# Kernel optimization log

Measured on AMD Instinct MI355X. Metric: run time of the kernel, lower is better.

Reference implementation:

```python
import jax, jax.numpy as jnp
import numpy as np

LSTM_IN = 125
LSTM_H = 125
MLP_D_H = 512
N = 512


def _lstm_scan(x, Wih, Whh, bih, bhh):
    # x: (N, LSTM_IN); PyTorch gate order: i, f, g, o
    H = LSTM_H
    def step(carry, xt):
        h, c = carry
        g = Wih @ xt + Whh @ h + bih + bhh  # (4H,)
        i = jax.nn.sigmoid(g[:H])
        f = jax.nn.sigmoid(g[H:2 * H])
        gg = jnp.tanh(g[2 * H:3 * H])
        o = jax.nn.sigmoid(g[3 * H:])
        c = f * c + i * gg
        h = o * jnp.tanh(c)
        return (h, c), h
    init = (jnp.zeros((H,), x.dtype), jnp.zeros((H,), x.dtype))
    _, hs = jax.lax.scan(step, init, x)
    return hs  # (N, H)


def setup_inputs() -> dict:
    key = jax.random.key(0)
    ks = jax.random.split(key, 14)
    s = 0.05
    d = {
        "sentence_emb": jax.random.normal(ks[0], (N, 1, LSTM_IN), jnp.float32),
        "Wih_f": jax.random.normal(ks[1], (4 * LSTM_H, LSTM_IN), jnp.float32) * s,
        "Whh_f": jax.random.normal(ks[2], (4 * LSTM_H, LSTM_H), jnp.float32) * s,
        "bih_f": jax.random.normal(ks[3], (4 * LSTM_H,), jnp.float32) * s,
        "bhh_f": jax.random.normal(ks[4], (4 * LSTM_H,), jnp.float32) * s,
        "Wih_b": jax.random.normal(ks[5], (4 * LSTM_H, LSTM_IN), jnp.float32) * s,
        "Whh_b": jax.random.normal(ks[6], (4 * LSTM_H, LSTM_H), jnp.float32) * s,
        "bih_b": jax.random.normal(ks[7], (4 * LSTM_H,), jnp.float32) * s,
        "bhh_b": jax.random.normal(ks[8], (4 * LSTM_H,), jnp.float32) * s,
        "W1": jax.random.normal(ks[9], (MLP_D_H, 4 * LSTM_H), jnp.float32) * s,
        "b1": jax.random.normal(ks[10], (MLP_D_H,), jnp.float32) * s,
        "W2": jax.random.normal(ks[11], (1, MLP_D_H), jnp.float32) * s,
        "b2": jax.random.normal(ks[12], (1,), jnp.float32) * s,
    }
    return d


def reference(sentence_emb, Wih_f, Whh_f, bih_f, bhh_f, Wih_b, Whh_b, bih_b, bhh_b, W1, b1, W2, b2):
    x = sentence_emb[:, 0, :]  # (N, 125), batch=1
    h_fwd = _lstm_scan(x, Wih_f, Whh_f, bih_f, bhh_f)           # (N, 125)
    h_bwd = _lstm_scan(x[::-1], Wih_b, Whh_b, bih_b, bhh_b)[::-1]  # (N, 125)
    h = jnp.concatenate([h_fwd, h_bwd], axis=-1)  # (N, 250)
    # output_mtx[i, j] = MLP(concat(h[j], h[i]))
    # Decompose first linear: W1 @ cat(h_j, h_i) = Wa @ h_j + Wb @ h_i
    D = h.shape[-1]
    Pa = h @ W1[:, :D].T   # (N, H): contribution of h_j
    Pb = h @ W1[:, D:].T   # (N, H): contribution of h_i
    hidden = jnp.tanh(Pb[:, None, :] + Pa[None, :, :] + b1)  # (N, N, H)
    out = hidden @ W2[0] + b2[0]  # (N, N)
    return out
```

## Files before the change

### kernel.cpp

```cpp
#include <hip/hip_runtime.h>

typedef __bf16 bf16_t;
typedef __bf16 bf16x8 __attribute__((ext_vector_type(8)));
typedef float f32x4 __attribute__((ext_vector_type(4)));
typedef int   int4v __attribute__((ext_vector_type(4)));

#define LOG2E 1.4426950408889634f

template<int CTRL>
__device__ __forceinline__ float qperm(float x) {
  return __builtin_bit_cast(float,
      __builtin_amdgcn_update_dpp(0, __builtin_bit_cast(int, x), CTRL, 0xF, 0xF, true));
}

__device__ __forceinline__ void lds_barrier() {
  asm volatile("s_waitcnt lgkmcnt(0)\n\ts_barrier" ::: "memory");
}

#if __has_builtin(__builtin_amdgcn_sdot4)
__device__ __forceinline__ int DOT4(int a, int b, int c) {
  return __builtin_amdgcn_sdot4(a, b, c, false);
}
#else
__device__ __forceinline__ int DOT4(int a, int b, int c) {
  #pragma unroll
  for (int i = 0; i < 4; ++i)
    c += ((a << (24 - 8 * i)) >> 24) * ((b << (24 - 8 * i)) >> 24);
  return c;
}
#endif

__global__ __launch_bounds__(256) void pre_kernel(
    const float* __restrict__ x,
    const float* __restrict__ Wih_f, const float* __restrict__ bih_f,
    const float* __restrict__ bhh_f,
    const float* __restrict__ Wih_b, const float* __restrict__ bih_b,
    const float* __restrict__ bhh_b,
    float* __restrict__ preT)
{
  const int dir = blockIdx.x >> 5;
  const int T   = blockIdx.x & 31;
  const float* __restrict__ Wih = dir ? Wih_b : Wih_f;
  const float* __restrict__ bih = dir ? bih_b : bih_f;
  const float* __restrict__ bhh = dir ? bhh_b : bhh_f;

  const int tid = threadIdx.x;
  const int wv  = tid >> 6;
  const int lane = tid & 63;
  const int q = lane >> 4, cc = lane & 15;

  const int r  = 16 * T + cc;
  const int na = r >> 2, pa = r & 3;
  const bool vld = (na < 125);
  const float* __restrict__ Wr = Wih + (vld ? (125 * pa + na) * 125 : 0);

  bf16x8 whi[4], wlo[4];
  #pragma unroll
  for (int ks = 0; ks < 4; ++ks) {
    #pragma unroll
    for (int j = 0; j < 8; ++j) {
      int k = 32 * ks + 8 * q + j;
      float wvv = (vld && k < 125) ? Wr[k] : 0.0f;
      bf16_t hi = (bf16_t)wvv;
      whi[ks][j] = hi;
      wlo[ks][j] = (bf16_t)(wvv - (float)hi);
    }
  }

  float bias[4];
  #pragma unroll
  for (int reg = 0; reg < 4; ++reg) {
    int ro = 16 * T + 4 * q + reg;
    int no = ro >> 2, po = ro & 3;
    bias[reg] = (no < 125) ? (bih[125 * po + no] + bhh[125 * po + no]) : 0.0f;
  }

  for (int i = 0; i < 8; ++i) {
    const int tt = 8 * wv + i;
    const int t  = 16 * tt + cc;
    const int trow = dir ? (511 - t) : t;
    const float* __restrict__ xr = x + trow * 125;

    f32x4 acc = (f32x4)0.0f;
    #pragma unroll
    for (int ks = 0; ks < 4; ++ks) {
      bf16x8 xhi, xlo;
      #pragma unroll
      for (int j = 0; j < 8; ++j) {
        int k = 32 * ks + 8 * q + j;
        float xv = (k < 125) ? xr[k] : 0.0f;
        bf16_t hi = (bf16_t)xv;
        xhi[j] = hi;
        xlo[j] = (bf16_t)(xv - (float)hi);
      }
      acc = __builtin_amdgcn_mfma_f32_16x16x32_bf16(whi[ks], xhi, acc, 0, 0, 0);
      acc = __builtin_amdgcn_mfma_f32_16x16x32_bf16(whi[ks], xlo, acc, 0, 0, 0);
      acc = __builtin_amdgcn_mfma_f32_16x16x32_bf16(wlo[ks], xhi, acc, 0, 0, 0);
    }
    #pragma unroll
    for (int reg = 0; reg < 4; ++reg) {
      int ro = 16 * T + 4 * q + reg;
      preT[dir * 262144 + ro * 512 + 16 * tt + cc] = acc[reg] + bias[reg];
    }
  }
}

__global__ __launch_bounds__(512) void lstm_kernel(
    const float* __restrict__ Whh_f, const float* __restrict__ Whh_b,
    const float* __restrict__ pre,
    bf16_t* __restrict__ h_all)
{
  const int dir = blockIdx.x;
  const float* __restrict__ Whh = dir ? Whh_b : Whh_f;

  const int tid  = threadIdx.x;
  const int lane = tid & 63;
  const int w    = tid >> 6;
  const int n    = tid >> 2;
  const int p    = tid & 3;
  const bool vld = (n < 125);
  const float* __restrict__ Wrow = Whh + (vld ? (125 * p + n) * 125 : 0);

  float m0 = 0.f, m1 = 0.f, m2 = 0.f, m3 = 0.f;
  if (vld) {
    #pragma unroll 4
    for (int k = 0; k < 124; k += 4) {
      m0 = fmaxf(m0, fabsf(Wrow[k + 0]));
      m1 = fmaxf(m1, fabsf(Wrow[k + 1]));
      m2 = fmaxf(m2, fabsf(Wrow[k + 2]));
      m3 = fmaxf(m3, fabsf(Wrow[k + 3]));
    }
    m0 = fmaxf(m0, fabsf(Wrow[124]));
  }
  float wm = fmaxf(fmaxf(m0, m1), fmaxf(m2, m3));
  #pragma unroll
  for (int off = 1; off < 64; off <<= 1)
    wm = fmaxf(wm, __shfl_xor(wm, off));
  __shared__ float wmx[8];
  if (lane == 0) wmx[w] = wm;
  __syncthreads();
  float wmax = wmx[0];
  #pragma unroll
  for (int u = 1; u < 8; ++u) wmax = fmaxf(wmax, wmx[u]);
  const float s_w  = 127.0f / wmax;
  const float invq = wmax / (127.0f * 127.0f);

  int wq[32];
  #pragma unroll
  for (int word = 0; word < 32; ++word) {
    int b = 0;
    #pragma unroll
    for (int byte = 0; byte < 4; ++byte) {
      int k = 4 * word + byte;
      int qv = 0;
      if (vld && k < 125)
        qv = (int)__builtin_rintf(Wrow[k] * s_w);
      b |= (qv & 0xFF) << (8 * byte);
    }
    wq[word] = b;
  }

  __shared__ __align__(16) char hbuf[2][128];
  if (tid < 256) ((char*)hbuf)[tid] = 0;
  if (dir == 0) {
    #pragma unroll
    for (int u = 0; u < 6; ++u) h_all[tid * 256 + 250 + u] = (bf16_t)0.0f;
  }
  __syncthreads();

  const float mult   = (p == 2) ? (-2.0f * LOG2E) : (-LOG2E);
  const float sA     = (p == 2) ? 2.0f : 1.0f;
  const float sB     = (p == 2) ? -1.0f : 0.0f;
  const float dscale = mult * invq;
  const float* __restrict__ preR = pre + dir * 262144 + tid * 512;
  float c = 0.0f;

  float4 pv_cur = *(const float4*)preR;

  for (int g = 0; g < 128; ++g) {
    float4 pv_nxt = make_float4(0.f, 0.f, 0.f, 0.f);
    if (g < 127) pv_nxt = *(const float4*)(preR + 4 * (g + 1));

    #pragma unroll
    for (int s4 = 0; s4 < 4; ++s4) {
      const int step = 4 * g + s4;
      const int cur  = s4 & 1, nxt = cur ^ 1;
      const float pv = (s4 == 0) ? pv_cur.x : (s4 == 1) ? pv_cur.y
                     : (s4 == 2) ? pv_cur.z : pv_cur.w;
      const float pvm = mult * pv;

      int hv[32];
      #pragma unroll
      for (int j = 0; j < 8; ++j) {
        int4v v = *(const int4v*)&hbuf[cur][16 * j];
        hv[4 * j + 0] = v[0];
        hv[4 * j + 1] = v[1];
        hv[4 * j + 2] = v[2];
        hv[4 * j + 3] = v[3];
      }

      int d0 = 0, d1 = 0, d2 = 0, d3 = 0;
      #pragma unroll
      for (int j = 0; j < 8; ++j) {
        d0 = DOT4(wq[4 * j + 0], hv[4 * j + 0], d0);
        d1 = DOT4(wq[4 * j + 1], hv[4 * j + 1], d1);
        d2 = DOT4(wq[4 * j + 2], hv[4 * j + 2], d2);
        d3 = DOT4(wq[4 * j + 3], hv[4 * j + 3], d3);
      }
      const int D = (d0 + d1) + (d2 + d3);

      float gf  = (float)D;
      float xg  = fmaf(gf, dscale, pvm);
      float e   = __builtin_amdgcn_exp2f(xg);
      float y   = __builtin_amdgcn_rcpf(1.0f + e);
      float act = fmaf(y, sA, sB);

      float b_i = qperm<0x00>(act);
      float b_f = qperm<0x55>(act);
      float b_g = qperm<0xAA>(act);
      float b_o = qperm<0xFF>(act);
      c = fmaf(b_f, c, b_i * b_g);
      float e2 = __builtin_amdgcn_exp2f(-2.0f * LOG2E * c);
      float tc = fmaf(__builtin_amdgcn_rcpf(1.0f + e2), 2.0f, -1.0f);
      float h  = b_o * tc;

      if (p == 0) {
        int qh = (int)__builtin_rintf(h * 127.0f);
        hbuf[nxt][n] = (char)qh;
        if (n < 125) {
          int t_orig = dir ? (511 - step) : step;
          h_all[t_orig * 256 + dir * 125 + n] = (bf16_t)h;
        }
      }
      lds_barrier();
    }
    pv_cur = pv_nxt;
  }
}

__global__ __launch_bounds__(256) void qgemm_kernel(
    const bf16_t* __restrict__ h_all,
    const float* __restrict__ W1,
    const float* __restrict__ b1,
    float* __restrict__ Qa,
    float* __restrict__ Qb)
{
  const int tid  = threadIdx.x;
  const int wv   = tid >> 6;
  const int lane = tid & 63;
  const int q    = lane >> 4, cc = lane & 15;
  const int bj   = blockIdx.x & 31;
  const int bm   = blockIdx.x >> 5;
  const int m    = bm * 64 + wv * 16 + cc;
  const int j0   = bj * 16;
  const int jA   = j0 + cc;

  const bool isB = (m >= 512);
  const int  row = isB ? (m - 512) : m;
  const int  cof = isB ? 250 : 0;

  f32x4 acc = (f32x4)0.0f;
  #pragma unroll
  for (int ks = 0; ks < 8; ++ks) {
    int kb = 32 * ks + 8 * q;
    bf16x8 a = *(const bf16x8*)&h_all[jA * 256 + kb];
    bf16x8 b;
    #pragma unroll
    for (int jj = 0; jj < 8; ++jj) {
      int k = kb + jj;
      float v = (k < 250) ? W1[row * 500 + cof + k] : 0.0f;
      b[jj] = (bf16_t)v;
    }
    acc = __builtin_amdgcn_mfma_f32_16x16x32_bf16(a, b, acc, 0, 0, 0);
  }

  const float C2 = 2.0f * LOG2E;
  #pragma unroll
  for (int reg = 0; reg < 4; ++reg) {
    int j = j0 + 4 * q + reg;
    float v = acc[reg];
    if (!isB) Qa[j * 512 + m] = C2 * v;
    else      Qb[j * 512 + (m - 512)] = C2 * (v + b1[m - 512]);
  }
}

__global__ __launch_bounds__(256) void outer_kernel(
    const float* __restrict__ Qa, const float* __restrict__ Qb,
    const float* __restrict__ W2, const float* __restrict__ b2,
    float* __restrict__ out)
{
  __shared__ float sa[2][32][33];
  __shared__ float sb[2][32][33];
  __shared__ float sw[2][32];

  const int tid = threadIdx.x;
  const int bi  = blockIdx.x >> 4, bjx = blockIdx.x & 15;
  const int i0  = bi * 32, j0 = bjx * 32;
  const int ii0 = (tid & 15) * 2;
  const int jj0 = (tid >> 4) * 2;
  const int ljj = tid & 31, kk4 = (tid >> 5) * 4;

  float accR[2][2] = {{0.0f, 0.0f}, {0.0f, 0.0f}};
  float wsum = 0.0f;

  for (int kc = 0; kc < 16; ++kc) {
    const int buf = kc & 1;
    const int k0  = kc * 32;
    float4 va = *(const float4*)&Qa[(j0 + ljj) * 512 + k0 + kk4];
    float4 vb = *(const float4*)&Qb[(i0 + ljj) * 512 + k0 + kk4];
    sa[buf][kk4 + 0][ljj] = va.x; sa[buf][kk4 + 1][ljj] = va.y;
    sa[buf][kk4 + 2][ljj] = va.z; sa[buf][kk4 + 3][ljj] = va.w;
    sb[buf][kk4 + 0][ljj] = vb.x; sb[buf][kk4 + 1][ljj] = vb.y;
    sb[buf][kk4 + 2][ljj] = vb.z; sb[buf][kk4 + 3][ljj] = vb.w;
    if (tid < 32) sw[buf][tid] = W2[k0 + tid];
    __syncthreads();

    #pragma unroll 4
    for (int kk = 0; kk < 32; ++kk) {
      float2 av = *(const float2*)&sa[buf][kk][jj0];
      float2 bv = *(const float2*)&sb[buf][kk][ii0];
      float wk = sw[buf][kk];
      wsum += wk;
      {
        float e = __builtin_amdgcn_exp2f(av.x + bv.x);
        accR[0][0] = fmaf(wk, __builtin_amdgcn_rcpf(1.0f + e), accR[0][0]);
      }
      {
        float e = __builtin_amdgcn_exp2f(av.y + bv.x);
        accR[0][1] = fmaf(wk, __builtin_amdgcn_rcpf(1.0f + e), accR[0][1]);
      }
      {
        float e = __builtin_amdgcn_exp2f(av.x + bv.y);
        accR[1][0] = fmaf(wk, __builtin_amdgcn_rcpf(1.0f + e), accR[1][0]);
      }
      {
        float e = __builtin_amdgcn_exp2f(av.y + bv.y);
        accR[1][1] = fmaf(wk, __builtin_amdgcn_rcpf(1.0f + e), accR[1][1]);
      }
    }
  }

  const float bb = b2[0];
  #pragma unroll
  for (int i2 = 0; i2 < 2; ++i2)
    #pragma unroll
    for (int j2 = 0; j2 < 2; ++j2)
      out[(i0 + ii0 + i2) * 512 + (j0 + jj0 + j2)] =
          wsum - 2.0f * accR[i2][j2] + bb;
}

extern "C" void kernel_launch(void* const* d_in, const int* in_sizes, int n_in,
                              void* d_out, int out_size, void* d_ws, size_t ws_size,
                              hipStream_t stream) {
  const float* emb   = (const float*)d_in[0];
  const float* Wih_f = (const float*)d_in[1];
  const float* Whh_f = (const float*)d_in[2];
  const float* bih_f = (const float*)d_in[3];
  const float* bhh_f = (const float*)d_in[4];
  const float* Wih_b = (const float*)d_in[5];
  const float* Whh_b = (const float*)d_in[6];
  const float* bih_b = (const float*)d_in[7];
  const float* bhh_b = (const float*)d_in[8];
  const float* W1    = (const float*)d_in[9];
  const float* b1    = (const float*)d_in[10];
  const float* W2    = (const float*)d_in[11];
  const float* b2    = (const float*)d_in[12];
  float* out = (float*)d_out;

  char* ws = (char*)d_ws;
  float*  pre   = (float*)ws;
  bf16_t* h_all = (bf16_t*)(ws + 2 * 1024 * 1024);
  float*  Qa    = (float*)(ws + 2 * 1024 * 1024 + 256 * 1024);
  float*  Qb    = Qa + 512 * 512;

  pre_kernel<<<64, 256, 0, stream>>>(emb, Wih_f, bih_f, bhh_f,
                                     Wih_b, bih_b, bhh_b, pre);
  lstm_kernel<<<2, 512, 0, stream>>>(Whh_f, Whh_b, pre, h_all);
  qgemm_kernel<<<512, 256, 0, stream>>>(h_all, W1, b1, Qa, Qb);
  outer_kernel<<<256, 256, 0, stream>>>(Qa, Qb, W2, b2, out);
}
```

Before: 378.7 us.

## Split LSTM recurrent dot products across quad lanes by K-slice with DPP reduction

Each quad of lanes now owns one hidden unit, and each lane holds a 32-element K-slice of all four gate rows instead of one full 125-element gate row. Per step a lane reads only 32 bytes of h from LDS instead of 128. The partial sums for the four gates are combined with a two-stage DPP butterfly, after which each lane ends up with its own gate's total. This is meant to cut per-step LDS traffic and the redundant broadcast reads on the serial critical path, at the cost of extra DPP and select instructions.

```diff
diff --git a/kernel.cpp b/kernel.cpp
--- a/kernel.cpp
+++ b/kernel.cpp
@@ -11,6 +11,11 @@
 __device__ __forceinline__ float qperm(float x) {
   return __builtin_bit_cast(float,
       __builtin_amdgcn_update_dpp(0, __builtin_bit_cast(int, x), CTRL, 0xF, 0xF, true));
+}
+
+template<int CTRL>
+__device__ __forceinline__ int iperm(int x) {
+  return __builtin_amdgcn_update_dpp(0, x, CTRL, 0xF, 0xF, true);
 }
 
 __device__ __forceinline__ void lds_barrier() {
@@ -119,18 +124,21 @@
   const int n    = tid >> 2;
   const int p    = tid & 3;
   const bool vld = (n < 125);
-  const float* __restrict__ Wrow = Whh + (vld ? (125 * p + n) * 125 : 0);
+  const int  klim = (p == 3) ? 29 : 32;
 
   float m0 = 0.f, m1 = 0.f, m2 = 0.f, m3 = 0.f;
   if (vld) {
-    #pragma unroll 4
-    for (int k = 0; k < 124; k += 4) {
-      m0 = fmaxf(m0, fabsf(Wrow[k + 0]));
-      m1 = fmaxf(m1, fabsf(Wrow[k + 1]));
-      m2 = fmaxf(m2, fabsf(Wrow[k + 2]));
-      m3 = fmaxf(m3, fabsf(Wrow[k + 3]));
-    }
-    m0 = fmaxf(m0, fabsf(Wrow[124]));
+    #pragma unroll
+    for (int g4 = 0; g4 < 4; ++g4) {
+      const float* __restrict__ Wg = Whh + (125 * g4 + n) * 125 + 32 * p;
+      for (int j = 0; j + 3 < klim; j += 4) {
+        m0 = fmaxf(m0, fabsf(Wg[j + 0]));
+        m1 = fmaxf(m1, fabsf(Wg[j + 1]));
+        m2 = fmaxf(m2, fabsf(Wg[j + 2]));
+        m3 = fmaxf(m3, fabsf(Wg[j + 3]));
+      }
+      if (klim == 29) m0 = fmaxf(m0, fabsf(Wg[28]));
+    }
   }
   float wm = fmaxf(fmaxf(m0, m1), fmaxf(m2, m3));
   #pragma unroll
@@ -145,19 +153,23 @@
   const float s_w  = 127.0f / wmax;
   const float invq = wmax / (127.0f * 127.0f);
 
-  int wq[32];
-  #pragma unroll
-  for (int word = 0; word < 32; ++word) {
-    int b = 0;
-    #pragma unroll
-    for (int byte = 0; byte < 4; ++byte) {
-      int k = 4 * word + byte;
-      int qv = 0;
-      if (vld && k < 125)
-        qv = (int)__builtin_rintf(Wrow[k] * s_w);
-      b |= (qv & 0xFF) << (8 * byte);
-    }
-    wq[word] = b;
+  int wq[4][8];
+  #pragma unroll
+  for (int g4 = 0; g4 < 4; ++g4) {
+    const float* __restrict__ Wg = Whh + (vld ? (125 * g4 + n) * 125 : 0);
+    #pragma unroll
+    for (int word = 0; word < 8; ++word) {
+      int b = 0;
+      #pragma unroll
+      for (int byte = 0; byte < 4; ++byte) {
+        int k = 32 * p + 4 * word + byte;
+        int qv = 0;
+        if (vld && k < 125)
+          qv = (int)__builtin_rintf(Wg[k] * s_w);
+        b |= (qv & 0xFF) << (8 * byte);
+      }
+      wq[g4][word] = b;
+    }
   }
 
   __shared__ __align__(16) char hbuf[2][128];
@@ -172,6 +184,7 @@
   const float sA     = (p == 2) ? 2.0f : 1.0f;
   const float sB     = (p == 2) ? -1.0f : 0.0f;
   const float dscale = mult * invq;
+  const int   q0 = p & 1, q1 = p >> 1;
   const float* __restrict__ preR = pre + dir * 262144 + tid * 512;
   float c = 0.0f;
 
@@ -189,25 +202,34 @@
                      : (s4 == 2) ? pv_cur.z : pv_cur.w;
       const float pvm = mult * pv;
 
-      int hv[32];
-      #pragma unroll
-      for (int j = 0; j < 8; ++j) {
-        int4v v = *(const int4v*)&hbuf[cur][16 * j];
-        hv[4 * j + 0] = v[0];
-        hv[4 * j + 1] = v[1];
-        hv[4 * j + 2] = v[2];
-        hv[4 * j + 3] = v[3];
-      }
+      int4v h0 = *(const int4v*)&hbuf[cur][32 * p];
+      int4v h1 = *(const int4v*)&hbuf[cur][32 * p + 16];
 
       int d0 = 0, d1 = 0, d2 = 0, d3 = 0;
       #pragma unroll
-      for (int j = 0; j < 8; ++j) {
-        d0 = DOT4(wq[4 * j + 0], hv[4 * j + 0], d0);
-        d1 = DOT4(wq[4 * j + 1], hv[4 * j + 1], d1);
-        d2 = DOT4(wq[4 * j + 2], hv[4 * j + 2], d2);
-        d3 = DOT4(wq[4 * j + 3], hv[4 * j + 3], d3);
-      }
-      const int D = (d0 + d1) + (d2 + d3);
+      for (int j = 0; j < 4; ++j) {
+        d0 = DOT4(wq[0][j], h0[j], d0);
+        d1 = DOT4(wq[1][j], h0[j], d1);
+        d2 = DOT4(wq[2][j], h0[j], d2);
+        d3 = DOT4(wq[3][j], h0[j], d3);
+      }
+      #pragma unroll
+      for (int j = 0; j < 4; ++j) {
+        d0 = DOT4(wq[0][4 + j], h1[j], d0);
+        d1 = DOT4(wq[1][4 + j], h1[j], d1);
+        d2 = DOT4(wq[2][4 + j], h1[j], d2);
+        d3 = DOT4(wq[3][4 + j], h1[j], d3);
+      }
+
+      int x0 = q0 ? d1 : d0;
+      int x1 = q0 ? d3 : d2;
+      int y0 = q0 ? d0 : d1;
+      int y1 = q0 ? d2 : d3;
+      int a0 = x0 + iperm<0xB1>(y0);
+      int a1 = x1 + iperm<0xB1>(y1);
+      int xx = q1 ? a1 : a0;
+      int yy = q1 ? a0 : a1;
+      const int D = xx + iperm<0x4E>(yy);
 
       float gf  = (float)D;
       float xg  = fmaf(gf, dscale, pvm);
```

New measurement: 371.8 us. About the same (-1.8%).
